# Performance work log

Hardware: AMD Instinct MI355X
Metric: run time of the kernel (lower is better)

The kernel has to match this reference:

```python
import jax, jax.numpy as jnp
import numpy as np

# ---- static geometry (matches init_kwargs) ----
B, S, D = 2, 4096, 2048
H, HD = 32, 64                      # num_heads, head_dim
HGRID, WGRID = 64, 64               # canvas h_dim, w_dim
TH, TW = 8, 16                      # tile size (th*tw = 128)
KH, KW = 16, 32                     # window (kernel) size
NTH, NTW = HGRID // TH, WGRID // TW
T = NTH * NTW                       # 32 tiles
TN = TH * TW                        # 128 tokens per tile
KTH, KTW = KH // TH, KW // TW
K = KTH * KTW                       # 4 kv tiles per query tile
SCALE = 1.0 / np.sqrt(HD)


def _kv_tile_ids():
    # For each query tile, the K kv tiles inside its (clamped) sliding window.
    qt = np.arange(T)
    qh, qw = qt // NTW, qt % NTW
    lbh, rbh = KTH // 2, KTH // 2 + (KTH % 2 - 1)
    lbw, rbw = KTW // 2, KTW // 2 + (KTW % 2 - 1)
    ch = np.clip(qh, lbh, NTH - 1 - rbh)
    cw = np.clip(qw, lbw, NTW - 1 - rbw)
    hh = ch[:, None] - lbh + np.arange(KTH)          # [T, KTH]
    ww = cw[:, None] - lbw + np.arange(KTW)          # [T, KTW]
    return (hh[:, :, None] * NTW + ww[:, None, :]).reshape(T, K)

KV_TILES = jnp.asarray(_kv_tile_ids())  # [T, K] int


def _to_tiles(x):
    # [B, S, H, HD] (row-major h,w) -> [B, H, T, TN, HD] (tile-major)
    x = x.reshape(B, NTH, TH, NTW, TW, H, HD)
    x = x.transpose(0, 5, 1, 3, 2, 4, 6)  # B,H,nth,ntw,th,tw,hd
    return x.reshape(B, H, T, TN, HD)


def _from_tiles(x):
    # [B, H, T, TN, HD] -> [B, S, H*HD]
    x = x.reshape(B, H, NTH, NTW, TH, TW, HD)
    x = x.transpose(0, 2, 4, 3, 5, 1, 6)  # B,nth,th,ntw,tw,H,hd
    return x.reshape(B, S, H * HD)


def setup_inputs() -> dict:
    key = jax.random.key(0)
    ks = jax.random.split(key, 5)
    sw = 1.0 / np.sqrt(D)
    return {
        "hidden_states": jax.random.normal(ks[0], (B, S, D), jnp.float32),
        "Wq": jax.random.normal(ks[1], (D, D), jnp.float32) * sw,
        "Wk": jax.random.normal(ks[2], (D, D), jnp.float32) * sw,
        "Wv": jax.random.normal(ks[3], (D, D), jnp.float32) * sw,
        "Wo": jax.random.normal(ks[4], (D, D), jnp.float32) * sw,
    }


def reference(hidden_states, Wq, Wk, Wv, Wo):
    # projections (weights stored [in, out]; equivalent to nn.Linear math)
    q = _to_tiles((hidden_states @ Wq).reshape(B, S, H, HD))  # [B,H,T,TN,HD]
    k = _to_tiles((hidden_states @ Wk).reshape(B, S, H, HD))
    v = _to_tiles((hidden_states @ Wv).reshape(B, S, H, HD))

    # gather the K allowed kv tiles for every query tile (block-sparse pattern)
    kg = k[:, :, KV_TILES].reshape(B, H, T, K * TN, HD)  # [B,H,T,K*TN,HD]
    vg = v[:, :, KV_TILES].reshape(B, H, T, K * TN, HD)

    # dense attention within each block (all gathered tokens are valid)
    scores = jnp.einsum("bhtqd,bhtkd->bhtqk", q, kg) * SCALE
    attn = jax.nn.softmax(scores, axis=-1)
    o = jnp.einsum("bhtqk,bhtkd->bhtqd", attn, vg)  # [B,H,T,TN,HD]

    return _from_tiles(o) @ Wo  # [B, S, D]
```

## Files before the change

kernel.cpp:

```cpp
#include <hip/hip_runtime.h>

typedef __bf16 bf16;
typedef __attribute__((ext_vector_type(8))) __bf16 bf16x8;
typedef __attribute__((ext_vector_type(4))) __bf16 bf16x4;
typedef __attribute__((ext_vector_type(4))) float f32x4;

#define MFMA16(a, b, c) __builtin_amdgcn_mfma_f32_16x16x32_bf16((a), (b), (c), 0, 0, 0)

__device__ __forceinline__ void gload16(const void* g, void* lds) {
  __builtin_amdgcn_global_load_lds(
      (__attribute__((address_space(1))) unsigned int*)(unsigned long long)g,
      (__attribute__((address_space(3))) unsigned int*)lds, 16, 0, 0);
}

__device__ __forceinline__ void transpose_tile(const float* __restrict__ W,
                                               bf16* __restrict__ WT, int bid,
                                               float (*tile)[65]) {
  int n0 = (bid & 31) * 64;
  int k0 = (bid >> 5) * 64;
  int tid = threadIdx.x;
  int r = tid >> 4;
  int c4 = (tid & 15) * 4;
#pragma unroll
  for (int i = 0; i < 4; ++i) {
    f32x4 v = *(const f32x4*)(W + (size_t)(k0 + r + i * 16) * 2048 + n0 + c4);
    tile[r + i * 16][c4 + 0] = v[0];
    tile[r + i * 16][c4 + 1] = v[1];
    tile[r + i * 16][c4 + 2] = v[2];
    tile[r + i * 16][c4 + 3] = v[3];
  }
  __syncthreads();
#pragma unroll
  for (int i = 0; i < 4; ++i) {
    int n = r + i * 16;
    bf16x4 o;
    o[0] = (bf16)tile[c4 + 0][n];
    o[1] = (bf16)tile[c4 + 1][n];
    o[2] = (bf16)tile[c4 + 2][n];
    o[3] = (bf16)tile[c4 + 3][n];
    *(bf16x4*)(WT + (size_t)(n0 + n) * 2048 + k0 + c4) = o;
  }
}

__global__ void __launch_bounds__(256) prep_kernel(const float* __restrict__ X,
                                                   const float* __restrict__ Wq,
                                                   const float* __restrict__ Wk,
                                                   const float* __restrict__ Wv,
                                                   bf16* __restrict__ Xb,
                                                   bf16* __restrict__ T0,
                                                   bf16* __restrict__ T1,
                                                   bf16* __restrict__ T2) {
  __shared__ float tile[64][65];
  int bid = blockIdx.x;
  if (bid < 3072) {
    int which = bid >> 10;
    const float* W = which == 0 ? Wq : (which == 1 ? Wk : Wv);
    bf16* WT = which == 0 ? T0 : (which == 1 ? T1 : T2);
    transpose_tile(W, WT, bid & 1023, tile);
  } else {
    size_t i = ((size_t)(bid - 3072) * 256 + threadIdx.x) * 8;
    f32x4 v0 = *(const f32x4*)(X + i);
    f32x4 v1 = *(const f32x4*)(X + i + 4);
    bf16x8 o;
    o[0] = (bf16)v0[0]; o[1] = (bf16)v0[1]; o[2] = (bf16)v0[2]; o[3] = (bf16)v0[3];
    o[4] = (bf16)v1[0]; o[5] = (bf16)v1[1]; o[6] = (bf16)v1[2]; o[7] = (bf16)v1[3];
    *(bf16x8*)(Xb + i) = o;
  }
}

__device__ __forceinline__ void gemm256_core(const bf16* __restrict__ Ag,
                                             const bf16* __restrict__ Bg,
                                             char* lds, f32x4 (&acc)[8][4]) {
  const int tid = threadIdx.x;
  const int lane = tid & 63, wid = tid >> 6;
  const int g = lane >> 4, r16 = lane & 15;
  const int wm = wid >> 2, wn = wid & 3;
  const int swz = ((g ^ ((r16 >> 1) & 3)) << 4);

  const int srow = wid * 32 + (lane >> 2);
  const int scol = ((lane & 3) ^ ((lane >> 3) & 3)) * 8;
  const bf16* gA = Ag + (size_t)srow * 2048 + scol;
  const bf16* gB = Bg + (size_t)srow * 2048 + scol;
  char* sA = lds + wid * 2048;
  char* sB = lds + 16384 + wid * 2048;

  const int arow0 = wm * 128 + r16;
  const int brow0 = wn * 64 + r16;

#define STAGE(bf_, tt_)                                                  \
  {                                                                      \
    char* dA_ = sA + (bf_) * 32768;                                      \
    const bf16* sA_ = gA + (size_t)(tt_) * 32;                           \
    gload16(sA_, dA_);                                                   \
    gload16(sA_ + (size_t)16 * 2048, dA_ + 1024);                        \
    char* dB_ = sB + (bf_) * 32768;                                      \
    const bf16* sB_ = gB + (size_t)(tt_) * 32;                           \
    gload16(sB_, dB_);                                                   \
    gload16(sB_ + (size_t)16 * 2048, dB_ + 1024);                        \
  }

#define READF(fa_, fb_, base_)                                           \
  {                                                                      \
    const char* Ab_ = lds + (base_);                                     \
    const char* Bb_ = Ab_ + 16384;                                       \
    _Pragma("unroll") for (int j_ = 0; j_ < 4; ++j_)                     \
      fb_[j_] = *(const bf16x8*)(Bb_ + (brow0 + j_ * 16) * 64 + swz);    \
    _Pragma("unroll") for (int i_ = 0; i_ < 8; ++i_)                     \
      fa_[i_] = *(const bf16x8*)(Ab_ + (arow0 + i_ * 16) * 64 + swz);    \
  }

#define MF(fa_, fb_)                                                     \
  {                                                                      \
    _Pragma("unroll") for (int i_ = 0; i_ < 8; ++i_)                     \
    _Pragma("unroll") for (int j_ = 0; j_ < 4; ++j_)                     \
      acc[i_][j_] = MFMA16(fa_[i_], fb_[j_], acc[i_][j_]);               \
  }

#define VMCHAIN(u_)                                                      \
  if ((u_) <= 60)      { asm volatile("s_waitcnt vmcnt(4)" ::: "memory"); } \
  else if ((u_) == 61) { asm volatile("s_waitcnt vmcnt(0)" ::: "memory"); }

  bf16x8 fA0[8], fB0[4], fA1[8], fB1[4];

  STAGE(0, 0) STAGE(1, 1) STAGE(2, 2)
  asm volatile("s_waitcnt vmcnt(4)" ::: "memory");
  __builtin_amdgcn_s_barrier();
  READF(fA0, fB0, 0)

  for (int t = 0; t < 64; t += 2) {
    if (t + 3 < 64) STAGE((t + 3) & 3, t + 3)
    VMCHAIN(t)
    READF(fA1, fB1, (size_t)((t + 1) & 3) * 32768)
    __builtin_amdgcn_sched_barrier(0);
    MF(fA0, fB0)
    __builtin_amdgcn_s_barrier();
    __builtin_amdgcn_sched_barrier(0);
    if (t + 4 < 64) STAGE((t + 4) & 3, t + 4)
    VMCHAIN(t + 1)
    READF(fA0, fB0, (size_t)((t + 2) & 3) * 32768)
    __builtin_amdgcn_sched_barrier(0);
    MF(fA1, fB1)
    __builtin_amdgcn_s_barrier();
    __builtin_amdgcn_sched_barrier(0);
  }
#undef STAGE
#undef READF
#undef MF
#undef VMCHAIN
}

__global__ void __launch_bounds__(512, 2) gemm_qkv_kernel(
    const bf16* __restrict__ Xb, const bf16* __restrict__ W0, const bf16* __restrict__ W1,
    const bf16* __restrict__ W2, bf16* __restrict__ q_t, bf16* __restrict__ k_t,
    bf16* __restrict__ v_t) {
  __shared__ char lds[131072];
  int bid = blockIdx.x;
  int xcd = bid & 7, idx = bid >> 3;
  int by = xcd * 4 + idx / 24, bx = idx % 24;
  int which = bx >> 3;
  int m0 = by * 256, n0 = (bx & 7) * 256;
  const bf16* W = which == 0 ? W0 : (which == 1 ? W1 : W2);

  f32x4 acc[8][4] = {};
  gemm256_core(Xb + (size_t)m0 * 2048, W + (size_t)n0 * 2048, lds, acc);

  int lane = threadIdx.x & 63, wid = threadIdx.x >> 6;
  int g = lane >> 4, r16 = lane & 15;
  int wm = wid >> 2, wn = wid & 3;
#pragma unroll
  for (int i = 0; i < 8; ++i) {
#pragma unroll
    for (int r = 0; r < 4; ++r) {
      int m = m0 + wm * 128 + i * 16 + g * 4 + r;
      int b = m >> 12, s = m & 4095;
      int hg = s >> 6, wg = s & 63;
      int t = ((hg >> 3) << 2) + (wg >> 4);
      int tn = ((hg & 7) << 4) + (wg & 15);
#pragma unroll
      for (int j = 0; j < 4; ++j) {
        int n = n0 + wn * 64 + j * 16 + r16;
        int h = n >> 6, hd = n & 63;
        float val = acc[i][j][r];
        size_t base = ((size_t)(b * 32 + h) * 32 + t);
        if (which == 0)
          q_t[(base * 128 + tn) * 64 + hd] = (bf16)(val * 0.18033688056680255f);
        else if (which == 1)
          k_t[(base * 128 + tn) * 64 + hd] = (bf16)val;
        else
          v_t[(base * 64 + hd) * 128 + tn] = (bf16)val;
      }
    }
  }
}

__global__ void __launch_bounds__(512, 2) gemm_out_kernel(const bf16* __restrict__ A,
                                                          const bf16* __restrict__ W,
                                                          float* __restrict__ C) {
  __shared__ char lds[131072];
  int bid = blockIdx.x;
  int xcd = bid & 7, idx = bid >> 3;
  int by = xcd * 4 + idx / 8, bx = idx & 7;
  int m0 = by * 256, n0 = bx * 256;

  f32x4 acc[8][4] = {};
  gemm256_core(A + (size_t)m0 * 2048, W + (size_t)n0 * 2048, lds, acc);

  int lane = threadIdx.x & 63, wid = threadIdx.x >> 6;
  int g = lane >> 4, r16 = lane & 15;
  int wm = wid >> 2, wn = wid & 3;
#pragma unroll
  for (int i = 0; i < 8; ++i)
#pragma unroll
    for (int j = 0; j < 4; ++j)
#pragma unroll
      for (int r = 0; r < 4; ++r) {
        int m = m0 + wm * 128 + i * 16 + g * 4 + r;
        int n = n0 + wn * 64 + j * 16 + r16;
        C[(size_t)m * 2048 + n] = acc[i][j][r];
      }
}

__global__ void __launch_bounds__(256) attn_kernel(const bf16* __restrict__ q_t,
                                                   const bf16* __restrict__ k_t,
                                                   const bf16* __restrict__ v_t,
                                                   bf16* __restrict__ o_bf,
                                                   const float* __restrict__ Wo,
                                                   bf16* __restrict__ WoT) {
  __shared__ char Pl[128 * 256];
  int bid = blockIdx.x;
  if (bid >= 2048) {
    transpose_tile(Wo, WoT, bid - 2048, (float(*)[65])Pl);
    return;
  }
  int bh = (bid & 7) * 8 + (bid >> 8);
  int t = (bid >> 3) & 31;
  int h = bh & 31, b = bh >> 5;
  int tid = threadIdx.x, w = tid >> 6, lane = tid & 63;
  int g = lane >> 4, r16 = lane & 15;

  const size_t qoff = ((size_t)bh * 32 + t) * (128 * 64);
  bf16x8 qf[2][2];
#pragma unroll
  for (int mf = 0; mf < 2; ++mf)
#pragma unroll
    for (int kf = 0; kf < 2; ++kf)
      qf[mf][kf] = *(const bf16x8*)&q_t[qoff + (size_t)(w * 32 + mf * 16 + r16) * 64 + kf * 32 + g * 8];

  bf16x8 ones;
#pragma unroll
  for (int j = 0; j < 8; ++j) ones[j] = (bf16)1.0f;

  f32x4 oacc[2][4] = {};
  f32x4 lacc[2] = {};

  int qh = t >> 2, qw = t & 3;
  int ch = qh < 1 ? 1 : (qh > 7 ? 7 : qh);
  int cw = qw < 1 ? 1 : (qw > 3 ? 3 : qw);

  for (int c = 0; c < 4; ++c) {
    int vt = (ch - 1 + (c >> 1)) * 4 + (cw - 1 + (c & 1));
    const bf16* Kt = k_t + ((size_t)bh * 32 + vt) * (128 * 64);
    const bf16* Vt = v_t + ((size_t)bh * 32 + vt) * (128 * 64);

    f32x4 s[2][8];
#pragma unroll
    for (int nf = 0; nf < 8; ++nf) {
      bf16x8 kf0 = *(const bf16x8*)&Kt[(nf * 16 + r16) * 64 + g * 8];
      bf16x8 kf1 = *(const bf16x8*)&Kt[(nf * 16 + r16) * 64 + 32 + g * 8];
#pragma unroll
      for (int mf = 0; mf < 2; ++mf) {
        f32x4 z = {};
        z = MFMA16(qf[mf][0], kf0, z);
        z = MFMA16(qf[mf][1], kf1, z);
        s[mf][nf] = z;
      }
    }

#pragma unroll
    for (int mf = 0; mf < 2; ++mf)
#pragma unroll
      for (int r = 0; r < 4; ++r) {
        int row = w * 32 + mf * 16 + g * 4 + r;
        int rb = row * 256;
        int swzp = (row & 7) << 4;
#pragma unroll
        for (int nf = 0; nf < 8; ++nf) {
          int addr = (rb + (nf * 16 + r16) * 2) ^ swzp;
          *(bf16*)(Pl + addr) = (bf16)__builtin_amdgcn_exp2f(s[mf][nf][r]);
        }
      }
    __builtin_amdgcn_sched_barrier(0);

#pragma unroll
    for (int ks = 0; ks < 4; ++ks) {
      bf16x8 pf[2];
#pragma unroll
      for (int mf = 0; mf < 2; ++mf) {
        int row = w * 32 + mf * 16 + r16;
        int addr = (row * 256 + ks * 64 + g * 16) ^ ((row & 7) << 4);
        pf[mf] = *(const bf16x8*)(Pl + addr);
      }
      bf16x8 vf[4];
#pragma unroll
      for (int hf = 0; hf < 4; ++hf)
        vf[hf] = *(const bf16x8*)&Vt[(hf * 16 + r16) * 128 + ks * 32 + g * 8];
#pragma unroll
      for (int mf = 0; mf < 2; ++mf) {
        lacc[mf] = MFMA16(pf[mf], ones, lacc[mf]);
#pragma unroll
        for (int hf = 0; hf < 4; ++hf)
          oacc[mf][hf] = MFMA16(pf[mf], vf[hf], oacc[mf][hf]);
      }
    }
    __builtin_amdgcn_sched_barrier(0);
  }

  int nth = t >> 2, ntw = t & 3;
#pragma unroll
  for (int mf = 0; mf < 2; ++mf)
#pragma unroll
    for (int r = 0; r < 4; ++r) {
      float inv = __builtin_amdgcn_rcpf(lacc[mf][r]);
      int tn = w * 32 + mf * 16 + g * 4 + r;
      int stok = (nth * 8 + (tn >> 4)) * 64 + ntw * 16 + (tn & 15);
#pragma unroll
      for (int hf = 0; hf < 4; ++hf) {
        int col = h * 64 + hf * 16 + r16;
        o_bf[((size_t)b * 4096 + stok) * 2048 + col] = (bf16)(oacc[mf][hf][r] * inv);
      }
    }
}

extern "C" void kernel_launch(void* const* d_in, const int* in_sizes, int n_in,
                              void* d_out, int out_size, void* d_ws, size_t ws_size,
                              hipStream_t stream) {
  const float* X = (const float*)d_in[0];
  const float* Wq = (const float*)d_in[1];
  const float* Wk = (const float*)d_in[2];
  const float* Wv = (const float*)d_in[3];
  const float* Wo = (const float*)d_in[4];
  float* out = (float*)d_out;
  char* ws = (char*)d_ws;
  if (ws_size < 159383552u) return;

  bf16* Xb  = (bf16*)(ws + 0);
  bf16* WT0 = (bf16*)(ws + 33554432u);
  bf16* WT1 = (bf16*)(ws + 41943040u);
  bf16* WT2 = (bf16*)(ws + 50331648u);
  bf16* q_t = (bf16*)(ws + 58720256u);
  bf16* k_t = (bf16*)(ws + 92274688u);
  bf16* v_t = (bf16*)(ws + 125829120u);
  bf16* o_bf = Xb;

  prep_kernel<<<11264, 256, 0, stream>>>(X, Wq, Wk, Wv, Xb, WT0, WT1, WT2);
  gemm_qkv_kernel<<<768, 512, 0, stream>>>(Xb, WT0, WT1, WT2, q_t, k_t, v_t);
  attn_kernel<<<3072, 256, 0, stream>>>(q_t, k_t, v_t, o_bf, Wo, WT0);
  gemm_out_kernel<<<256, 512, 0, stream>>>(o_bf, WT0, out);
}
```

Before: 436.9 us.

## Load GEMM B operand directly from global into registers, halve LDS footprint

The shared GEMM core stops staging the weight (B) tile through LDS. Each wave now loads its B fragments straight from global memory into registers, double-buffered across k-steps, while only A is staged in a 4-slot LDS ring. LDS per block drops from 128 KB to 64 KB, which can let two 512-thread blocks fit per CU and removes the B-side LDS traffic. In exchange the four waves sharing a column block each fetch the same B data, adding redundant global/L2 traffic. The explicit vmcnt wait chain is also dropped, so load completion inside the loop is left to compiler-inserted waits.

Measured after the change: 647.7 us. +48.3%, slower.

```diff
diff --git a/kernel.cpp b/kernel.cpp
--- a/kernel.cpp
+++ b/kernel.cpp
@@ -80,31 +80,30 @@
   const int srow = wid * 32 + (lane >> 2);
   const int scol = ((lane & 3) ^ ((lane >> 3) & 3)) * 8;
   const bf16* gA = Ag + (size_t)srow * 2048 + scol;
-  const bf16* gB = Bg + (size_t)srow * 2048 + scol;
   char* sA = lds + wid * 2048;
-  char* sB = lds + 16384 + wid * 2048;
+
+  const bf16* gBF = Bg + (size_t)(wn * 64 + r16) * 2048 + g * 8;
 
   const int arow0 = wm * 128 + r16;
-  const int brow0 = wn * 64 + r16;
-
-#define STAGE(bf_, tt_)                                                  \
+
+#define STAGE_A(sl_, tt_)                                                \
   {                                                                      \
-    char* dA_ = sA + (bf_) * 32768;                                      \
-    const bf16* sA_ = gA + (size_t)(tt_) * 32;                           \
-    gload16(sA_, dA_);                                                   \
-    gload16(sA_ + (size_t)16 * 2048, dA_ + 1024);                        \
-    char* dB_ = sB + (bf_) * 32768;                                      \
-    const bf16* sB_ = gB + (size_t)(tt_) * 32;                           \
-    gload16(sB_, dB_);                                                   \
-    gload16(sB_ + (size_t)16 * 2048, dB_ + 1024);                        \
-  }
-
-#define READF(fa_, fb_, base_)                                           \
+    char* d_ = sA + (sl_) * 16384;                                       \
+    const bf16* s_ = gA + (size_t)(tt_) * 32;                            \
+    gload16(s_, d_);                                                     \
+    gload16(s_ + (size_t)16 * 2048, d_ + 1024);                          \
+  }
+
+#define BLOAD(dst_, tt_)                                                 \
   {                                                                      \
-    const char* Ab_ = lds + (base_);                                     \
-    const char* Bb_ = Ab_ + 16384;                                       \
     _Pragma("unroll") for (int j_ = 0; j_ < 4; ++j_)                     \
-      fb_[j_] = *(const bf16x8*)(Bb_ + (brow0 + j_ * 16) * 64 + swz);    \
+      dst_[j_] = *(const bf16x8*)(gBF + (size_t)j_ * 16 * 2048 +         \
+                                  (size_t)(tt_) * 32);                   \
+  }
+
+#define READF_A(fa_, sl_)                                                \
+  {                                                                      \
+    const char* Ab_ = lds + (sl_) * 16384;                               \
     _Pragma("unroll") for (int i_ = 0; i_ < 8; ++i_)                     \
       fa_[i_] = *(const bf16x8*)(Ab_ + (arow0 + i_ * 16) * 64 + swz);    \
   }
@@ -116,44 +115,40 @@
       acc[i_][j_] = MFMA16(fa_[i_], fb_[j_], acc[i_][j_]);               \
   }
 
-#define VMCHAIN(u_)                                                      \
-  if ((u_) <= 60)      { asm volatile("s_waitcnt vmcnt(4)" ::: "memory"); } \
-  else if ((u_) == 61) { asm volatile("s_waitcnt vmcnt(0)" ::: "memory"); }
-
-  bf16x8 fA0[8], fB0[4], fA1[8], fB1[4];
-
-  STAGE(0, 0) STAGE(1, 1) STAGE(2, 2)
-  asm volatile("s_waitcnt vmcnt(4)" ::: "memory");
+  bf16x8 fA[8], bB0[4], bB1[4];
+
+  STAGE_A(0, 0) STAGE_A(1, 1)
+  BLOAD(bB0, 0)
+  asm volatile("s_waitcnt vmcnt(6)" ::: "memory");
   __builtin_amdgcn_s_barrier();
-  READF(fA0, fB0, 0)
 
   for (int t = 0; t < 64; t += 2) {
-    if (t + 3 < 64) STAGE((t + 3) & 3, t + 3)
-    VMCHAIN(t)
-    READF(fA1, fB1, (size_t)((t + 1) & 3) * 32768)
-    __builtin_amdgcn_sched_barrier(0);
-    MF(fA0, fB0)
+    READF_A(fA, t & 3)
+    if (t + 2 < 64) STAGE_A((t + 2) & 3, t + 2)
+    if (t + 1 < 64) BLOAD(bB1, t + 1)
+    __builtin_amdgcn_sched_barrier(0);
+    MF(fA, bB0)
     __builtin_amdgcn_s_barrier();
     __builtin_amdgcn_sched_barrier(0);
-    if (t + 4 < 64) STAGE((t + 4) & 3, t + 4)
-    VMCHAIN(t + 1)
-    READF(fA0, fB0, (size_t)((t + 2) & 3) * 32768)
-    __builtin_amdgcn_sched_barrier(0);
-    MF(fA1, fB1)
+    READF_A(fA, (t + 1) & 3)
+    if (t + 3 < 64) STAGE_A((t + 3) & 3, t + 3)
+    if (t + 2 < 64) BLOAD(bB0, t + 2)
+    __builtin_amdgcn_sched_barrier(0);
+    MF(fA, bB1)
     __builtin_amdgcn_s_barrier();
     __builtin_amdgcn_sched_barrier(0);
   }
-#undef STAGE
-#undef READF
+#undef STAGE_A
+#undef BLOAD
+#undef READF_A
 #undef MF
-#undef VMCHAIN
 }
 
 __global__ void __launch_bounds__(512, 2) gemm_qkv_kernel(
     const bf16* __restrict__ Xb, const bf16* __restrict__ W0, const bf16* __restrict__ W1,
     const bf16* __restrict__ W2, bf16* __restrict__ q_t, bf16* __restrict__ k_t,
     bf16* __restrict__ v_t) {
-  __shared__ char lds[131072];
+  __shared__ char lds[65536];
   int bid = blockIdx.x;
   int xcd = bid & 7, idx = bid >> 3;
   int by = xcd * 4 + idx / 24, bx = idx % 24;
@@ -196,7 +191,7 @@
 __global__ void __launch_bounds__(512, 2) gemm_out_kernel(const bf16* __restrict__ A,
                                                           const bf16* __restrict__ W,
                                                           float* __restrict__ C) {
-  __shared__ char lds[131072];
+  __shared__ char lds[65536];
   int bid = blockIdx.x;
   int xcd = bid & 7, idx = bid >> 3;
   int by = xcd * 4 + idx / 8, bx = idx & 7;
```
